# Kernel optimization log

Measured on AMD Instinct MI355X. Metric: run time of the kernel, lower is better.

Reference implementation:

```python
import jax, jax.numpy as jnp
import numpy as np

D_MODEL = 1024
N_HEADS = 16


def setup_inputs() -> dict:
    key = jax.random.key(0)
    ks = jax.random.split(key, 5)
    b, t, d = 4, 2048, D_MODEL
    x = jax.random.normal(ks[0], (b, t, d), dtype=jnp.float32)
    s = 1.0 / np.sqrt(d)
    qkv_w = jax.random.normal(ks[1], (d, 3 * d), dtype=jnp.float32) * s
    qkv_b = jnp.zeros((3 * d,), dtype=jnp.float32)
    o_w = jax.random.normal(ks[2], (d, d), dtype=jnp.float32) * s
    o_b = jnp.zeros((d,), dtype=jnp.float32)
    return {"x": x, "qkv_w": qkv_w, "qkv_b": qkv_b, "o_w": o_w, "o_b": o_b}


def reference(x, qkv_w, qkv_b, o_w, o_b):
    b, t, d = x.shape
    h = N_HEADS
    hd = d // h
    qkv = x @ qkv_w + qkv_b  # [b, t, 3d]
    q, k, v = jnp.split(qkv, 3, axis=-1)
    # [b, h, t, hd]
    q = q.reshape(b, t, h, hd).transpose(0, 2, 1, 3)
    k = k.reshape(b, t, h, hd).transpose(0, 2, 1, 3)
    v = v.reshape(b, t, h, hd).transpose(0, 2, 1, 3)
    scores = jnp.einsum("bhqd,bhkd->bhqk", q, k) / jnp.sqrt(jnp.float32(hd))
    causal = jnp.tril(jnp.ones((t, t), dtype=bool))
    scores = jnp.where(causal[None, None, :, :], scores, -jnp.inf)
    wts = jax.nn.softmax(scores, axis=-1)  # dropout p=0.0 -> identity
    y = jnp.einsum("bhqk,bhkd->bhqd", wts, v)
    y = y.transpose(0, 2, 1, 3).reshape(b, t, d)
    return y @ o_w + o_b
```

## Files before the change

### kernel.cpp

```cpp
#include <hip/hip_runtime.h>

typedef unsigned short ushort_t;
typedef __attribute__((ext_vector_type(8))) short short8;
typedef __attribute__((ext_vector_type(4))) float f32x4;
typedef __attribute__((ext_vector_type(4))) unsigned int uint4v;

__device__ __forceinline__ ushort_t f2bf(float f) {
  union { float f; unsigned int u; } v; v.f = f;
  unsigned int u = v.u;
  unsigned int r = (u + 0x7fffu + ((u >> 16) & 1u)) >> 16;
  return (ushort_t)r;
}

__device__ __forceinline__ unsigned int pk2(float hi, float lo) {
  union { float f; unsigned int u; } a, b; a.f = lo; b.f = hi;
  return __builtin_amdgcn_perm(b.u, a.u, 0x07060302u);
}

__device__ __forceinline__ void load_lds16(const void* g, void* l) {
  __builtin_amdgcn_global_load_lds(
      (const __attribute__((address_space(1))) unsigned int*)g,
      (__attribute__((address_space(3))) unsigned int*)l, 16, 0, 0);
}

__global__ __launch_bounds__(256) void cvt_f32_to_bf16_vec(
    const float* __restrict__ in, ushort_t* __restrict__ out, int n8) {
  int i = blockIdx.x * 256 + threadIdx.x;
  if (i >= n8) return;
  const float4* p = (const float4*)in;
  float4 a = p[2 * i];
  float4 b = p[2 * i + 1];
  short8 v;
  v[0] = (short)f2bf(a.x); v[1] = (short)f2bf(a.y);
  v[2] = (short)f2bf(a.z); v[3] = (short)f2bf(a.w);
  v[4] = (short)f2bf(b.x); v[5] = (short)f2bf(b.y);
  v[6] = (short)f2bf(b.z); v[7] = (short)f2bf(b.w);
  *(short8*)(out + (size_t)i * 8) = v;
}

__global__ __launch_bounds__(256) void transpose_to_bf16(
    const float* __restrict__ in, ushort_t* __restrict__ out, int R, int C) {
  __shared__ float tile[64][65];
  int c0 = blockIdx.x * 64, r0 = blockIdx.y * 64;
  int tid = threadIdx.x;
  for (int it = 0; it < 16; ++it) {
    int l = it * 256 + tid;
    int r = l >> 6, c = l & 63;
    tile[r][c] = in[(size_t)(r0 + r) * C + c0 + c];
  }
  __syncthreads();
  for (int it = 0; it < 16; ++it) {
    int l = it * 256 + tid;
    int ro = l >> 6, co = l & 63;
    out[(size_t)(c0 + ro) * R + r0 + co] = f2bf(tile[co][ro]);
  }
}

__device__ __forceinline__ void gemm_bt_main(
    const ushort_t* __restrict__ A, const ushort_t* __restrict__ Bt,
    int K, int bm, int bn, ushort_t* lds, f32x4 acc[4][4]) {
  const int tid = threadIdx.x;
  const int wave = tid >> 6, lane = tid & 63;
  const int quad = lane >> 4, col = lane & 15;
  const int wm = (wave & 1) * 64, wn = (wave >> 1) * 64;
  ushort_t* ldsA = lds;
  ushort_t* ldsB = lds + 8192;
  f32x4 z = {0.f, 0.f, 0.f, 0.f};
  for (int i = 0; i < 4; ++i)
    for (int j = 0; j < 4; ++j) acc[i][j] = z;
  for (int bk = 0; bk < K; bk += 64) {
    for (int is = 0; is < 4; ++is) {
      int o = is * 4096 + wave * 1024 + lane * 16;
      int p = o >> 13;
      int w = o & 8191;
      int r = w >> 6, kk = (w & 63) >> 1;
      int ldso = (is * 4096 + wave * 1024) >> 1;
      const ushort_t* ga = A + (size_t)(bm + r) * K + bk + p * 32 + kk;
      load_lds16(ga, ldsA + ldso);
      const ushort_t* gb = Bt + (size_t)(bn + r) * K + bk + p * 32 + kk;
      load_lds16(gb, ldsB + ldso);
    }
    __syncthreads();
    for (int ks = 0; ks < 2; ++ks) {
      short8 af[4], bfr[4];
      for (int i = 0; i < 4; ++i)
        af[i] = *(const short8*)(ldsA + ks * 4096 + (wm + i * 16 + col) * 32 + quad * 8);
      for (int j = 0; j < 4; ++j)
        bfr[j] = *(const short8*)(ldsB + ks * 4096 + (wn + j * 16 + col) * 32 + quad * 8);
      for (int i = 0; i < 4; ++i)
        for (int j = 0; j < 4; ++j)
          acc[i][j] = __builtin_amdgcn_mfma_f32_16x16x32_bf16(af[i], bfr[j], acc[i][j], 0, 0, 0);
    }
    __syncthreads();
  }
}

__global__ __launch_bounds__(256) void gemm_qkv(
    const ushort_t* __restrict__ Xb, const ushort_t* __restrict__ W1t,
    const float* __restrict__ bias, ushort_t* __restrict__ Qb,
    ushort_t* __restrict__ Kb, ushort_t* __restrict__ Vtb) {
  __shared__ ushort_t lds[16384];
  const int ntile = 3072 / 128;
  int bn = (blockIdx.x % ntile) * 128;
  int bm = (blockIdx.x / ntile) * 128;
  f32x4 acc[4][4];
  gemm_bt_main(Xb, W1t, 1024, bm, bn, lds, acc);
  const int tid = threadIdx.x, wave = tid >> 6, lane = tid & 63;
  const int quad = lane >> 4, col = lane & 15;
  const int wm = (wave & 1) * 64, wn = (wave >> 1) * 64;
  int which = bn >> 10;
  for (int i = 0; i < 4; ++i) {
    int row0 = bm + wm + i * 16 + quad * 4;
    int b = row0 >> 11, t0 = row0 & 2047;
    for (int j = 0; j < 4; ++j) {
      int cg = bn + wn + j * 16 + col;
      float bv = bias[cg];
      int rem = cg & 1023;
      int h = rem >> 6, hd = rem & 63;
      size_t bh = (size_t)(b * 16 + h);
      if (which == 0) {
        for (int r = 0; r < 4; ++r)
          Qb[(bh * 2048 + t0 + r) * 64 + hd] = f2bf(acc[i][j][r] + bv);
      } else if (which == 1) {
        for (int r = 0; r < 4; ++r)
          Kb[(bh * 2048 + t0 + r) * 64 + hd] = f2bf(acc[i][j][r] + bv);
      } else {
        ushort4 pk;
        pk.x = f2bf(acc[i][j][0] + bv);
        pk.y = f2bf(acc[i][j][1] + bv);
        pk.z = f2bf(acc[i][j][2] + bv);
        pk.w = f2bf(acc[i][j][3] + bv);
        *(ushort4*)(Vtb + (bh * 64 + hd) * 2048 + t0) = pk;
      }
    }
  }
}

__global__ __launch_bounds__(256) void gemm_out_k(
    const ushort_t* __restrict__ Yb, const ushort_t* __restrict__ W2t,
    const float* __restrict__ bias, float* __restrict__ out) {
  __shared__ ushort_t lds[16384];
  const int ntile = 1024 / 128;
  int bn = (blockIdx.x % ntile) * 128;
  int bm = (blockIdx.x / ntile) * 128;
  f32x4 acc[4][4];
  gemm_bt_main(Yb, W2t, 1024, bm, bn, lds, acc);
  const int tid = threadIdx.x, wave = tid >> 6, lane = tid & 63;
  const int quad = lane >> 4, col = lane & 15;
  const int wm = (wave & 1) * 64, wn = (wave >> 1) * 64;
  for (int i = 0; i < 4; ++i) {
    int row0 = bm + wm + i * 16 + quad * 4;
    for (int j = 0; j < 4; ++j) {
      int cg = bn + wn + j * 16 + col;
      float bv = bias[cg];
      for (int r = 0; r < 4; ++r)
        out[(size_t)(row0 + r) * 1024 + cg] = acc[i][j][r] + bv;
    }
  }
}

#define KS_OFF 0
#define VS_OFF 9216
__global__ __launch_bounds__(256) void attn(
    const ushort_t* __restrict__ Qb, const ushort_t* __restrict__ Kb,
    const ushort_t* __restrict__ Vtb, ushort_t* __restrict__ Yb) {
  __shared__ ushort_t lds[17920];
  const int tid = threadIdx.x, wave = tid >> 6, lane = tid & 63;
  const int quad = lane >> 4, col = lane & 15;
  int bh = blockIdx.x & 63;
  int qt = 15 - (blockIdx.x >> 6);
  int q0 = qt * 128;
  int b = bh >> 4, h = bh & 15;
  const ushort_t* Qg = Qb + (size_t)bh * 2048 * 64;
  const ushort_t* Kg = Kb + (size_t)bh * 2048 * 64;
  const ushort_t* Vg = Vtb + (size_t)bh * 64 * 2048;

  for (int it = 0; it < 4; ++it) {
    int v = it * 256 + tid;
    int r = v >> 3, co = (v & 7) * 8;
    short8 val = *(const short8*)(Qg + (size_t)(q0 + r) * 64 + co);
    *(short8*)(lds + KS_OFF + r * 72 + co) = val;
  }
  __syncthreads();
  short8 qf[2][2];
  for (int i = 0; i < 2; ++i)
    for (int ks = 0; ks < 2; ++ks)
      qf[i][ks] = *(const short8*)(lds + KS_OFF + (wave * 32 + i * 16 + col) * 72 + ks * 32 + quad * 8);

  f32x4 z = {0.f, 0.f, 0.f, 0.f};
  f32x4 oacc[2][4];
  float mst[2] = {-3.0e38f, -3.0e38f}, lst[2] = {0.f, 0.f};
  for (int i = 0; i < 2; ++i)
    for (int dt = 0; dt < 4; ++dt) oacc[i][dt] = z;
  const float CL = 0.18033688011112042f;

  for (int kt = 0; kt <= qt; ++kt) {
    int k0 = kt * 128;
    __syncthreads();
    for (int it = 0; it < 4; ++it) {
      int v = it * 256 + tid;
      int r = v >> 3, co = (v & 7) * 8;
      short8 val = *(const short8*)(Kg + (size_t)(k0 + r) * 64 + co);
      *(short8*)(lds + KS_OFF + r * 72 + co) = val;
    }
    for (int it = 0; it < 4; ++it) {
      int v = it * 256 + tid;
      int d = v >> 4, m = v & 15;
      int kc = m * 8;
      short8 val = *(const short8*)(Vg + (size_t)d * 2048 + k0 + kc);
      int p = kc >> 5, u = (kc >> 4) & 1, g0 = (kc >> 2) & 3;
      int pos1 = p * 32 + g0 * 8 + u * 4;
      ushort4 lo4, hi4;
      lo4.x = (ushort_t)val[0]; lo4.y = (ushort_t)val[1];
      lo4.z = (ushort_t)val[2]; lo4.w = (ushort_t)val[3];
      hi4.x = (ushort_t)val[4]; hi4.y = (ushort_t)val[5];
      hi4.z = (ushort_t)val[6]; hi4.w = (ushort_t)val[7];
      *(ushort4*)(lds + VS_OFF + d * 136 + pos1) = lo4;
      *(ushort4*)(lds + VS_OFF + d * 136 + pos1 + 8) = hi4;
    }
    __syncthreads();
    f32x4 s[2][8];
    for (int i = 0; i < 2; ++i)
      for (int j = 0; j < 8; ++j) s[i][j] = z;
    for (int j = 0; j < 8; ++j) {
      short8 kf0 = *(const short8*)(lds + KS_OFF + (j * 16 + col) * 72 + quad * 8);
      short8 kf1 = *(const short8*)(lds + KS_OFF + (j * 16 + col) * 72 + 32 + quad * 8);
      for (int i = 0; i < 2; ++i) {
        s[i][j] = __builtin_amdgcn_mfma_f32_16x16x32_bf16(kf0, qf[i][0], s[i][j], 0, 0, 0);
        s[i][j] = __builtin_amdgcn_mfma_f32_16x16x32_bf16(kf1, qf[i][1], s[i][j], 0, 0, 0);
      }
    }
    if (kt == qt) {
      for (int i = 0; i < 2; ++i) {
        int qg = q0 + wave * 32 + i * 16 + col;
        for (int j = 0; j < 8; ++j) {
          int kg = k0 + j * 16 + quad * 4;
          for (int r = 0; r < 4; ++r)
            if (kg + r > qg) s[i][j][r] = -3.0e38f;
        }
      }
    }
    for (int i = 0; i < 2; ++i) {
      f32x4 vm = s[i][0];
      for (int j = 1; j < 8; ++j)
        for (int r = 0; r < 4; ++r) vm[r] = fmaxf(vm[r], s[i][j][r]);
      float rm = fmaxf(fmaxf(vm[0], vm[1]), fmaxf(vm[2], vm[3]));
      rm = fmaxf(rm, __shfl_xor(rm, 16));
      rm = fmaxf(rm, __shfl_xor(rm, 32));
      float mnew = fmaxf(mst[i], rm);
      float alpha = __builtin_amdgcn_exp2f((mst[i] - mnew) * CL);
      mst[i] = mnew;
      float mb = mnew * CL;
      float rs = 0.f;
      for (int j = 0; j < 8; ++j)
        for (int r = 0; r < 4; ++r) {
          float p = __builtin_amdgcn_exp2f(fmaf(s[i][j][r], CL, -mb));
          s[i][j][r] = p;
          rs += p;
        }
      rs += __shfl_xor(rs, 16);
      rs += __shfl_xor(rs, 32);
      lst[i] = lst[i] * alpha + rs;
      for (int dt = 0; dt < 4; ++dt)
        for (int r = 0; r < 4; ++r) oacc[i][dt][r] *= alpha;
    }
    for (int p2 = 0; p2 < 4; ++p2) {
      short8 pf[2];
      for (int i = 0; i < 2; ++i) {
        uint4v w;
        w[0] = pk2(s[i][2 * p2][1], s[i][2 * p2][0]);
        w[1] = pk2(s[i][2 * p2][3], s[i][2 * p2][2]);
        w[2] = pk2(s[i][2 * p2 + 1][1], s[i][2 * p2 + 1][0]);
        w[3] = pk2(s[i][2 * p2 + 1][3], s[i][2 * p2 + 1][2]);
        pf[i] = *(short8*)&w;
      }
      for (int dt = 0; dt < 4; ++dt) {
        short8 vf = *(const short8*)(lds + VS_OFF + (dt * 16 + col) * 136 + p2 * 32 + quad * 8);
        for (int i = 0; i < 2; ++i)
          oacc[i][dt] = __builtin_amdgcn_mfma_f32_16x16x32_bf16(vf, pf[i], oacc[i][dt], 0, 0, 0);
      }
    }
  }
  for (int i = 0; i < 2; ++i) {
    float linv = 1.0f / lst[i];
    int t = q0 + wave * 32 + i * 16 + col;
    size_t base = ((size_t)(b * 2048 + t)) * 1024 + h * 64;
    for (int dt = 0; dt < 4; ++dt) {
      ushort4 pk;
      pk.x = f2bf(oacc[i][dt][0] * linv);
      pk.y = f2bf(oacc[i][dt][1] * linv);
      pk.z = f2bf(oacc[i][dt][2] * linv);
      pk.w = f2bf(oacc[i][dt][3] * linv);
      *(ushort4*)(Yb + base + dt * 16 + quad * 4) = pk;
    }
  }
}

extern "C" void kernel_launch(void* const* d_in, const int* in_sizes, int n_in,
                              void* d_out, int out_size, void* d_ws, size_t ws_size,
                              hipStream_t stream) {
  const float* x     = (const float*)d_in[0];
  const float* qkv_w = (const float*)d_in[1];
  const float* qkv_b = (const float*)d_in[2];
  const float* o_w   = (const float*)d_in[3];
  const float* o_b   = (const float*)d_in[4];
  float* out = (float*)d_out;
  char* ws = (char*)d_ws;
  ushort_t* Xb  = (ushort_t*)(ws);
  ushort_t* W1t = (ushort_t*)(ws + 16777216);
  ushort_t* W2t = (ushort_t*)(ws + 23068672);
  ushort_t* Qb  = (ushort_t*)(ws + 25165824);
  ushort_t* Kb  = (ushort_t*)(ws + 41943040);
  ushort_t* Vtb = (ushort_t*)(ws + 58720256);
  ushort_t* Yb  = Xb;

  cvt_f32_to_bf16_vec<<<4096, 256, 0, stream>>>(x, Xb, 1048576);
  transpose_to_bf16<<<dim3(48, 16), 256, 0, stream>>>(qkv_w, W1t, 1024, 3072);
  transpose_to_bf16<<<dim3(16, 16), 256, 0, stream>>>(o_w, W2t, 1024, 1024);
  gemm_qkv<<<1536, 256, 0, stream>>>(Xb, W1t, qkv_b, Qb, Kb, Vtb);
  attn<<<1024, 256, 0, stream>>>(Qb, Kb, Vtb, Yb);
  gemm_out_k<<<512, 256, 0, stream>>>(Yb, W2t, o_b, out);
}
```

Baseline: 286.4 us.

## Pair causal q-tiles per block, prefetch K/V into registers, fold softmax scale into Q

Each attention block now handles two query tiles (qt = 15-a and a), so every block does the same amount of causal work, and the grid is halved. The next K/V tile is loaded from global memory into registers while the current tile is being computed, overlapping global latency with MFMA work. The softmax scale times log2(e) is applied to Q in the QKV GEMM epilogue, which removes the per-score multiply in the exp2 path. Q fragments are read straight from global memory instead of staged through LDS, and launch bounds ask for 2 blocks per CU. The costs are extra register pressure from the prefetch buffers and bf16 rounding of the pre-scaled Q.

After: 258.4 us. -9.8%, faster.

```diff
diff --git a/kernel.cpp b/kernel.cpp
--- a/kernel.cpp
+++ b/kernel.cpp
@@ -108,6 +108,7 @@
   const int tid = threadIdx.x, wave = tid >> 6, lane = tid & 63;
   const int quad = lane >> 4, col = lane & 15;
   const int wm = (wave & 1) * 64, wn = (wave >> 1) * 64;
+  const float SCL = 0.18033688011112042f;
   int which = bn >> 10;
   for (int i = 0; i < 4; ++i) {
     int row0 = bm + wm + i * 16 + quad * 4;
@@ -120,7 +121,7 @@
       size_t bh = (size_t)(b * 16 + h);
       if (which == 0) {
         for (int r = 0; r < 4; ++r)
-          Qb[(bh * 2048 + t0 + r) * 64 + hd] = f2bf(acc[i][j][r] + bv);
+          Qb[(bh * 2048 + t0 + r) * 64 + hd] = f2bf((acc[i][j][r] + bv) * SCL);
       } else if (which == 1) {
         for (int r = 0; r < 4; ++r)
           Kb[(bh * 2048 + t0 + r) * 64 + hd] = f2bf(acc[i][j][r] + bv);
@@ -161,137 +162,148 @@
 
 #define KS_OFF 0
 #define VS_OFF 9216
-__global__ __launch_bounds__(256) void attn(
+__global__ __launch_bounds__(256, 2) void attn(
     const ushort_t* __restrict__ Qb, const ushort_t* __restrict__ Kb,
     const ushort_t* __restrict__ Vtb, ushort_t* __restrict__ Yb) {
   __shared__ ushort_t lds[17920];
   const int tid = threadIdx.x, wave = tid >> 6, lane = tid & 63;
   const int quad = lane >> 4, col = lane & 15;
-  int bh = blockIdx.x & 63;
-  int qt = 15 - (blockIdx.x >> 6);
-  int q0 = qt * 128;
-  int b = bh >> 4, h = bh & 15;
+  const int bh = blockIdx.x & 63;
+  const int a = blockIdx.x >> 6;
+  const int b = bh >> 4, h = bh & 15;
   const ushort_t* Qg = Qb + (size_t)bh * 2048 * 64;
   const ushort_t* Kg = Kb + (size_t)bh * 2048 * 64;
   const ushort_t* Vg = Vtb + (size_t)bh * 64 * 2048;
-
-  for (int it = 0; it < 4; ++it) {
-    int v = it * 256 + tid;
-    int r = v >> 3, co = (v & 7) * 8;
-    short8 val = *(const short8*)(Qg + (size_t)(q0 + r) * 64 + co);
-    *(short8*)(lds + KS_OFF + r * 72 + co) = val;
-  }
-  __syncthreads();
-  short8 qf[2][2];
-  for (int i = 0; i < 2; ++i)
-    for (int ks = 0; ks < 2; ++ks)
-      qf[i][ks] = *(const short8*)(lds + KS_OFF + (wave * 32 + i * 16 + col) * 72 + ks * 32 + quad * 8);
-
+  const int kv = tid;
   f32x4 z = {0.f, 0.f, 0.f, 0.f};
-  f32x4 oacc[2][4];
-  float mst[2] = {-3.0e38f, -3.0e38f}, lst[2] = {0.f, 0.f};
-  for (int i = 0; i < 2; ++i)
-    for (int dt = 0; dt < 4; ++dt) oacc[i][dt] = z;
-  const float CL = 0.18033688011112042f;
-
-  for (int kt = 0; kt <= qt; ++kt) {
-    int k0 = kt * 128;
-    __syncthreads();
+
+  for (int item = 0; item < 2; ++item) {
+    const int qt = item == 0 ? 15 - a : a;
+    const int q0 = qt * 128;
+    short8 qf[2][2];
+    for (int i = 0; i < 2; ++i)
+      for (int ks = 0; ks < 2; ++ks)
+        qf[i][ks] = *(const short8*)(
+            Qg + (size_t)(q0 + wave * 32 + i * 16 + col) * 64 + ks * 32 + quad * 8);
+    short8 kpre[4], vpre[4];
+#pragma unroll
     for (int it = 0; it < 4; ++it) {
-      int v = it * 256 + tid;
-      int r = v >> 3, co = (v & 7) * 8;
-      short8 val = *(const short8*)(Kg + (size_t)(k0 + r) * 64 + co);
-      *(short8*)(lds + KS_OFF + r * 72 + co) = val;
-    }
-    for (int it = 0; it < 4; ++it) {
-      int v = it * 256 + tid;
-      int d = v >> 4, m = v & 15;
-      int kc = m * 8;
-      short8 val = *(const short8*)(Vg + (size_t)d * 2048 + k0 + kc);
-      int p = kc >> 5, u = (kc >> 4) & 1, g0 = (kc >> 2) & 3;
-      int pos1 = p * 32 + g0 * 8 + u * 4;
-      ushort4 lo4, hi4;
-      lo4.x = (ushort_t)val[0]; lo4.y = (ushort_t)val[1];
-      lo4.z = (ushort_t)val[2]; lo4.w = (ushort_t)val[3];
-      hi4.x = (ushort_t)val[4]; hi4.y = (ushort_t)val[5];
-      hi4.z = (ushort_t)val[6]; hi4.w = (ushort_t)val[7];
-      *(ushort4*)(lds + VS_OFF + d * 136 + pos1) = lo4;
-      *(ushort4*)(lds + VS_OFF + d * 136 + pos1 + 8) = hi4;
-    }
-    __syncthreads();
-    f32x4 s[2][8];
+      int v = it * 256 + kv;
+      kpre[it] = *(const short8*)(Kg + (size_t)(0 + (v >> 3)) * 64 + (v & 7) * 8);
+      vpre[it] = *(const short8*)(Vg + (size_t)(v >> 4) * 2048 + 0 + (v & 15) * 8);
+    }
+
+    f32x4 oacc[2][4];
+    float mst[2] = {-3.0e38f, -3.0e38f}, lst[2] = {0.f, 0.f};
     for (int i = 0; i < 2; ++i)
-      for (int j = 0; j < 8; ++j) s[i][j] = z;
-    for (int j = 0; j < 8; ++j) {
-      short8 kf0 = *(const short8*)(lds + KS_OFF + (j * 16 + col) * 72 + quad * 8);
-      short8 kf1 = *(const short8*)(lds + KS_OFF + (j * 16 + col) * 72 + 32 + quad * 8);
+      for (int dt = 0; dt < 4; ++dt) oacc[i][dt] = z;
+
+    for (int kt = 0; kt <= qt; ++kt) {
+      int k0 = kt * 128;
+      __syncthreads();
+#pragma unroll
+      for (int it = 0; it < 4; ++it) {
+        int v = it * 256 + kv;
+        *(short8*)(lds + KS_OFF + (v >> 3) * 72 + (v & 7) * 8) = kpre[it];
+      }
+#pragma unroll
+      for (int it = 0; it < 4; ++it) {
+        int v = it * 256 + kv;
+        int d = v >> 4, kc = (v & 15) * 8;
+        int p = kc >> 5, u = (kc >> 4) & 1, g0 = (kc >> 2) & 3;
+        int pos1 = p * 32 + g0 * 8 + u * 4;
+        short8 val = vpre[it];
+        ushort4 lo4, hi4;
+        lo4.x = (ushort_t)val[0]; lo4.y = (ushort_t)val[1];
+        lo4.z = (ushort_t)val[2]; lo4.w = (ushort_t)val[3];
+        hi4.x = (ushort_t)val[4]; hi4.y = (ushort_t)val[5];
+        hi4.z = (ushort_t)val[6]; hi4.w = (ushort_t)val[7];
+        *(ushort4*)(lds + VS_OFF + d * 136 + pos1) = lo4;
+        *(ushort4*)(lds + VS_OFF + d * 136 + pos1 + 8) = hi4;
+      }
+      __syncthreads();
+      if (kt < qt) {
+        int k0n = k0 + 128;
+#pragma unroll
+        for (int it = 0; it < 4; ++it) {
+          int v = it * 256 + kv;
+          kpre[it] = *(const short8*)(Kg + (size_t)(k0n + (v >> 3)) * 64 + (v & 7) * 8);
+          vpre[it] = *(const short8*)(Vg + (size_t)(v >> 4) * 2048 + k0n + (v & 15) * 8);
+        }
+      }
+      f32x4 s[2][8];
+      for (int i = 0; i < 2; ++i)
+        for (int j = 0; j < 8; ++j) s[i][j] = z;
+      for (int j = 0; j < 8; ++j) {
+        short8 kf0 = *(const short8*)(lds + KS_OFF + (j * 16 + col) * 72 + quad * 8);
+        short8 kf1 = *(const short8*)(lds + KS_OFF + (j * 16 + col) * 72 + 32 + quad * 8);
+        for (int i = 0; i < 2; ++i) {
+          s[i][j] = __builtin_amdgcn_mfma_f32_16x16x32_bf16(kf0, qf[i][0], s[i][j], 0, 0, 0);
+          s[i][j] = __builtin_amdgcn_mfma_f32_16x16x32_bf16(kf1, qf[i][1], s[i][j], 0, 0, 0);
+        }
+      }
+      if (kt == qt) {
+        for (int i = 0; i < 2; ++i) {
+          int qg = q0 + wave * 32 + i * 16 + col;
+          for (int j = 0; j < 8; ++j) {
+            int kg = k0 + j * 16 + quad * 4;
+            for (int r = 0; r < 4; ++r)
+              if (kg + r > qg) s[i][j][r] = -3.0e38f;
+          }
+        }
+      }
       for (int i = 0; i < 2; ++i) {
-        s[i][j] = __builtin_amdgcn_mfma_f32_16x16x32_bf16(kf0, qf[i][0], s[i][j], 0, 0, 0);
-        s[i][j] = __builtin_amdgcn_mfma_f32_16x16x32_bf16(kf1, qf[i][1], s[i][j], 0, 0, 0);
-      }
-    }
-    if (kt == qt) {
-      for (int i = 0; i < 2; ++i) {
-        int qg = q0 + wave * 32 + i * 16 + col;
-        for (int j = 0; j < 8; ++j) {
-          int kg = k0 + j * 16 + quad * 4;
-          for (int r = 0; r < 4; ++r)
-            if (kg + r > qg) s[i][j][r] = -3.0e38f;
+        f32x4 vm = s[i][0];
+        for (int j = 1; j < 8; ++j)
+          for (int r = 0; r < 4; ++r) vm[r] = fmaxf(vm[r], s[i][j][r]);
+        float rm = fmaxf(fmaxf(vm[0], vm[1]), fmaxf(vm[2], vm[3]));
+        rm = fmaxf(rm, __shfl_xor(rm, 16));
+        rm = fmaxf(rm, __shfl_xor(rm, 32));
+        float mnew = fmaxf(mst[i], rm);
+        float alpha = __builtin_amdgcn_exp2f(mst[i] - mnew);
+        mst[i] = mnew;
+        float rs = 0.f;
+        for (int j = 0; j < 8; ++j)
+          for (int r = 0; r < 4; ++r) {
+            float p = __builtin_amdgcn_exp2f(s[i][j][r] - mnew);
+            s[i][j][r] = p;
+            rs += p;
+          }
+        rs += __shfl_xor(rs, 16);
+        rs += __shfl_xor(rs, 32);
+        lst[i] = lst[i] * alpha + rs;
+        for (int dt = 0; dt < 4; ++dt)
+          for (int r = 0; r < 4; ++r) oacc[i][dt][r] *= alpha;
+      }
+      for (int p2 = 0; p2 < 4; ++p2) {
+        short8 pf[2];
+        for (int i = 0; i < 2; ++i) {
+          uint4v w;
+          w[0] = pk2(s[i][2 * p2][1], s[i][2 * p2][0]);
+          w[1] = pk2(s[i][2 * p2][3], s[i][2 * p2][2]);
+          w[2] = pk2(s[i][2 * p2 + 1][1], s[i][2 * p2 + 1][0]);
+          w[3] = pk2(s[i][2 * p2 + 1][3], s[i][2 * p2 + 1][2]);
+          pf[i] = *(short8*)&w;
+        }
+        for (int dt = 0; dt < 4; ++dt) {
+          short8 vf = *(const short8*)(lds + VS_OFF + (dt * 16 + col) * 136 + p2 * 32 + quad * 8);
+          for (int i = 0; i < 2; ++i)
+            oacc[i][dt] = __builtin_amdgcn_mfma_f32_16x16x32_bf16(vf, pf[i], oacc[i][dt], 0, 0, 0);
         }
       }
     }
     for (int i = 0; i < 2; ++i) {
-      f32x4 vm = s[i][0];
-      for (int j = 1; j < 8; ++j)
-        for (int r = 0; r < 4; ++r) vm[r] = fmaxf(vm[r], s[i][j][r]);
-      float rm = fmaxf(fmaxf(vm[0], vm[1]), fmaxf(vm[2], vm[3]));
-      rm = fmaxf(rm, __shfl_xor(rm, 16));
-      rm = fmaxf(rm, __shfl_xor(rm, 32));
-      float mnew = fmaxf(mst[i], rm);
-      float alpha = __builtin_amdgcn_exp2f((mst[i] - mnew) * CL);
-      mst[i] = mnew;
-      float mb = mnew * CL;
-      float rs = 0.f;
-      for (int j = 0; j < 8; ++j)
-        for (int r = 0; r < 4; ++r) {
-          float p = __builtin_amdgcn_exp2f(fmaf(s[i][j][r], CL, -mb));
-          s[i][j][r] = p;
-          rs += p;
-        }
-      rs += __shfl_xor(rs, 16);
-      rs += __shfl_xor(rs, 32);
-      lst[i] = lst[i] * alpha + rs;
-      for (int dt = 0; dt < 4; ++dt)
-        for (int r = 0; r < 4; ++r) oacc[i][dt][r] *= alpha;
-    }
-    for (int p2 = 0; p2 < 4; ++p2) {
-      short8 pf[2];
-      for (int i = 0; i < 2; ++i) {
-        uint4v w;
-        w[0] = pk2(s[i][2 * p2][1], s[i][2 * p2][0]);
-        w[1] = pk2(s[i][2 * p2][3], s[i][2 * p2][2]);
-        w[2] = pk2(s[i][2 * p2 + 1][1], s[i][2 * p2 + 1][0]);
-        w[3] = pk2(s[i][2 * p2 + 1][3], s[i][2 * p2 + 1][2]);
-        pf[i] = *(short8*)&w;
-      }
+      float linv = 1.0f / lst[i];
+      int t = q0 + wave * 32 + i * 16 + col;
+      size_t base = ((size_t)(b * 2048 + t)) * 1024 + h * 64;
       for (int dt = 0; dt < 4; ++dt) {
-        short8 vf = *(const short8*)(lds + VS_OFF + (dt * 16 + col) * 136 + p2 * 32 + quad * 8);
-        for (int i = 0; i < 2; ++i)
-          oacc[i][dt] = __builtin_amdgcn_mfma_f32_16x16x32_bf16(vf, pf[i], oacc[i][dt], 0, 0, 0);
-      }
-    }
-  }
-  for (int i = 0; i < 2; ++i) {
-    float linv = 1.0f / lst[i];
-    int t = q0 + wave * 32 + i * 16 + col;
-    size_t base = ((size_t)(b * 2048 + t)) * 1024 + h * 64;
-    for (int dt = 0; dt < 4; ++dt) {
-      ushort4 pk;
-      pk.x = f2bf(oacc[i][dt][0] * linv);
-      pk.y = f2bf(oacc[i][dt][1] * linv);
-      pk.z = f2bf(oacc[i][dt][2] * linv);
-      pk.w = f2bf(oacc[i][dt][3] * linv);
-      *(ushort4*)(Yb + base + dt * 16 + quad * 4) = pk;
+        ushort4 pk;
+        pk.x = f2bf(oacc[i][dt][0] * linv);
+        pk.y = f2bf(oacc[i][dt][1] * linv);
+        pk.z = f2bf(oacc[i][dt][2] * linv);
+        pk.w = f2bf(oacc[i][dt][3] * linv);
+        *(ushort4*)(Yb + base + dt * 16 + quad * 4) = pk;
+      }
     }
   }
 }
@@ -318,6 +330,6 @@
   transpose_to_bf16<<<dim3(48, 16), 256, 0, stream>>>(qkv_w, W1t, 1024, 3072);
   transpose_to_bf16<<<dim3(16, 16), 256, 0, stream>>>(o_w, W2t, 1024, 1024);
   gemm_qkv<<<1536, 256, 0, stream>>>(Xb, W1t, qkv_b, Qb, Kb, Vtb);
-  attn<<<1024, 256, 0, stream>>>(Qb, Kb, Vtb, Yb);
+  attn<<<512, 256, 0, stream>>>(Qb, Kb, Vtb, Yb);
   gemm_out_k<<<512, 256, 0, stream>>>(Yb, W2t, o_b, out);
 }
```
